# Optimization experiments

Measured on AMD Instinct MI355X. Metric: run time of the kernel, lower is better.

The kernel has to match this reference:

```python
import jax, jax.numpy as jnp
import numpy as np

WS = 7  # window_size

def idct_matrix(N, dtype=jnp.float32):
    # scipy.fftpack.idct type-2 (no norm): y[n] = x[0] + 2*sum_{k>=1} x[k] cos(pi*k*(2n+1)/(2N))
    n = jnp.arange(N, dtype=dtype)[:, None]
    k = jnp.arange(N, dtype=dtype)[None, :]
    M = 2.0 * jnp.cos(jnp.pi * (2.0 * n + 1.0) * k / (2.0 * N))
    return M.at[:, 0].set(1.0)

def setup_inputs() -> dict:
    key = jax.random.key(0)
    k1, k2 = jax.random.split(key)
    B, H, W = 8, 384, 384
    X = jax.random.normal(k1, (B, H, W, WS * WS - 1), dtype=jnp.float32)
    im_zero_freq = jax.random.normal(k2, (B, H, W, 1), dtype=jnp.float32)
    return {"X": X, "im_zero_freq": im_zero_freq}

def reference(X, im_zero_freq):
    B, H, W, _ = X.shape
    ws = WS
    P, Q = H - ws, W - ws  # loop ranges: range(H-ws), range(W-ws)
    # Patch coefficient vector at (i,j): [zero_freq, high_freq...] -> (ws, ws)
    coeff = jnp.concatenate([im_zero_freq[:, :P, :Q, :], X[:, :P, :Q, :]], axis=-1)
    coeff = coeff.reshape(B, P, Q, ws, ws)
    M = idct_matrix(ws).astype(X.dtype)
    # 2D IDCT (axis 1 then axis 2 of each patch) as two small matmuls
    patches = jnp.einsum('nu,mv,bpquv->bpqnm', M, M, coeff)  # [B,P,Q,ws,ws]
    # Overwrite semantics: pixel (y,x) keeps the value from the LAST patch that
    # covered it, i.e. patch (min(y,P-1), min(x,Q-1)). Rows/cols beyond H-2/W-2
    # are never written and stay zero.
    y = jnp.arange(H)
    x = jnp.arange(W)
    i_sel = jnp.minimum(y, P - 1)
    j_sel = jnp.minimum(x, Q - 1)
    dy = y - i_sel  # offset within the selected patch, in [0, ws-1]
    dx = x - j_sel
    out = patches[:, i_sel[:, None], j_sel[None, :], dy[:, None], dx[None, :]]  # [B,H,W]
    valid = (y[:, None] <= H - 2) & (x[None, :] <= W - 2)
    out = jnp.where(valid[None, :, :], out, jnp.zeros((), dtype=out.dtype))
    return out[..., None]  # [B,H,W,1]
```

## Files before the change

kernel.cpp:

```cpp
#include <hip/hip_runtime.h>

#define WS 7
#define BB 8
#define HH 384
#define WW 384
#define PP 377
#define NC 48
#define STRIDE 49
#define NSITE PP
#define NX4 (PP * 12)

__constant__ float d_M[49] = {
    1.0f,  1.9498558244f,  1.8019377358f,  1.5636629649f,  1.2469796037f,  0.8677674782f,  0.4450418679f,
    1.0f,  1.5636629649f,  0.4450418679f, -0.8677674782f, -1.8019377358f, -1.9498558244f, -1.2469796037f,
    1.0f,  0.8677674782f, -1.2469796037f, -1.9498558244f, -0.4450418679f,  1.5636629649f,  1.8019377358f,
    1.0f,  0.0f,          -2.0f,           0.0f,           2.0f,           0.0f,          -2.0f,
    1.0f, -0.8677674782f, -1.2469796037f,  1.9498558244f, -0.4450418679f, -1.5636629649f,  1.8019377358f,
    1.0f, -1.5636629649f,  0.4450418679f,  0.8677674782f, -1.8019377358f,  1.9498558244f, -1.2469796037f,
    1.0f, -1.9498558244f,  1.8019377358f, -1.5636629649f,  1.2469796037f, -0.8677674782f,  0.4450418679f,
};

__global__ __launch_bounds__(384) void idct_row_kernel(
    const float* __restrict__ X,
    const float* __restrict__ zf,
    float* __restrict__ out)
{
    __shared__ float lds[NSITE * STRIDE];
    __shared__ float ldsM[49];

    const int t   = threadIdx.x;
    const int row = blockIdx.x;
    const int y   = row % HH;
    const int b   = row / HH;

    const size_t obase = (size_t)row * WW;

    if (y == HH - 1) { out[obase + t] = 0.0f; return; }

    const int i = min(y, PP - 1);
    const size_t rbase = ((size_t)b * HH + i) * WW;
    const float4* __restrict__ xrow = (const float4*)(X + rbase * NC);

    if (t < 49) ldsM[t] = d_M[t];

    for (int q = t; q < NX4; q += 384) {
        float4 v = xrow[q];
        int j = q / 12;
        int m = q - j * 12;
        float* dst = &lds[j * STRIDE + 1 + 4 * m];
        dst[0] = v.x; dst[1] = v.y; dst[2] = v.z; dst[3] = v.w;
    }
    if (t < NSITE) lds[t * STRIDE] = zf[rbase + t];

    __syncthreads();

    const int x  = t;
    const int j  = min(x, PP - 1);
    const int dx = x - j;
    const int dy = y - i;

    const float* c  = &lds[j * STRIDE];
    const float* wu = &ldsM[dy * 7];
    const float* wv = &ldsM[dx * 7];

    float acc = 0.0f;
#pragma unroll
    for (int u = 0; u < 7; ++u) {
        float s = 0.0f;
#pragma unroll
        for (int v = 0; v < 7; ++v)
            s = fmaf(wv[v], c[u * 7 + v], s);
        acc = fmaf(wu[u], s, acc);
    }

    if (x == WW - 1) acc = 0.0f;
    out[obase + x] = acc;
}

extern "C" void kernel_launch(void* const* d_in, const int* in_sizes, int n_in,
                              void* d_out, int out_size, void* d_ws, size_t ws_size,
                              hipStream_t stream) {
    const float* X  = (const float*)d_in[0];
    const float* zf = (const float*)d_in[1];
    float* out = (float*)d_out;

    idct_row_kernel<<<BB * HH, 384, 0, stream>>>(X, zf, out);
}
```

Before: 340.9 us.

## Compute per-float4 partial dot products in registers instead of staging patches in LDS

Each thread now loads its twelve float4 chunks of the patch row into registers and multiplies them straight away with precomputed 2D IDCT weights (outer product of the row and column weight vectors for dx=0). Only 12 partial sums per site go to LDS instead of the full 49-coefficient patch, which cuts LDS traffic and bank conflicts. The final stage sums the partials per site. The few edge columns where dx>0 fall back to a direct global-memory computation. It adds extra global reads on the edge path and a second barrier.

After: 305.9 us. -10.3%, faster.

```diff
diff --git a/kernel.cpp b/kernel.cpp
--- a/kernel.cpp
+++ b/kernel.cpp
@@ -1,14 +1,10 @@
 #include <hip/hip_runtime.h>
 
-#define WS 7
-#define BB 8
 #define HH 384
 #define WW 384
 #define PP 377
 #define NC 48
-#define STRIDE 49
-#define NSITE PP
-#define NX4 (PP * 12)
+#define NX4R (PP * 12)
 
 __constant__ float d_M[49] = {
     1.0f,  1.9498558244f,  1.8019377358f,  1.5636629649f,  1.2469796037f,  0.8677674782f,  0.4450418679f,
@@ -20,60 +16,84 @@
     1.0f, -1.9498558244f,  1.8019377358f, -1.5636629649f,  1.2469796037f, -0.8677674782f,  0.4450418679f,
 };
 
-__global__ __launch_bounds__(384) void idct_row_kernel(
+__global__ __launch_bounds__(384) void idct_partial_kernel(
     const float* __restrict__ X,
     const float* __restrict__ zf,
     float* __restrict__ out)
 {
-    __shared__ float lds[NSITE * STRIDE];
-    __shared__ float ldsM[49];
+    __shared__ float w49[49];
+    __shared__ float part[PP * 13];
 
     const int t   = threadIdx.x;
     const int row = blockIdx.x;
     const int y   = row % HH;
     const int b   = row / HH;
-
     const size_t obase = (size_t)row * WW;
 
     if (y == HH - 1) { out[obase + t] = 0.0f; return; }
 
-    const int i = min(y, PP - 1);
+    const int i  = min(y, PP - 1);
+    const int dy = y - i;
     const size_t rbase = ((size_t)b * HH + i) * WW;
+
+    if (t < 49) w49[t] = d_M[dy * 7 + t / 7] * d_M[t % 7];
+    __syncthreads();
+
+    const int m  = t % 12;
+    const int s0 = t / 12;
+    const float wa = w49[1 + 4 * m];
+    const float wb = w49[2 + 4 * m];
+    const float wc = w49[3 + 4 * m];
+    const float wd = w49[4 + 4 * m];
+
     const float4* __restrict__ xrow = (const float4*)(X + rbase * NC);
 
-    if (t < 49) ldsM[t] = d_M[t];
-
-    for (int q = t; q < NX4; q += 384) {
-        float4 v = xrow[q];
-        int j = q / 12;
-        int m = q - j * 12;
-        float* dst = &lds[j * STRIDE + 1 + 4 * m];
-        dst[0] = v.x; dst[1] = v.y; dst[2] = v.z; dst[3] = v.w;
+    float4 v[12];
+#pragma unroll
+    for (int k = 0; k < 12; ++k) {
+        int q = t + 384 * k;
+        v[k] = xrow[q < NX4R ? q : (NX4R - 1)];
     }
-    if (t < NSITE) lds[t * STRIDE] = zf[rbase + t];
-
+#pragma unroll
+    for (int k = 0; k < 12; ++k) {
+        int q = t + 384 * k;
+        if (q < NX4R) {
+            float p = fmaf(v[k].x, wa, fmaf(v[k].y, wb, fmaf(v[k].z, wc, v[k].w * wd)));
+            part[(s0 + 32 * k) * 13 + m] = p;
+        }
+    }
     __syncthreads();
 
-    const int x  = t;
-    const int j  = min(x, PP - 1);
-    const int dx = x - j;
-    const int dy = y - i;
+    const int x = t;
+    const int j = min(x, PP - 1);
+    const float zv = zf[rbase + j];
+    float acc;
 
-    const float* c  = &lds[j * STRIDE];
-    const float* wu = &ldsM[dy * 7];
-    const float* wv = &ldsM[dx * 7];
-
-    float acc = 0.0f;
+    if (x < PP) {
+        const float* p = &part[j * 13];
+        float a0 = (p[0] + p[1]) + (p[2] + p[3]);
+        float a1 = (p[4] + p[5]) + (p[6] + p[7]);
+        float a2 = (p[8] + p[9]) + (p[10] + p[11]);
+        acc = zv + (a0 + a1) + a2;
+    } else if (x == WW - 1) {
+        acc = 0.0f;
+    } else {
+        const int dx = x - (PP - 1);
+        const float* __restrict__ c = X + (rbase + (PP - 1)) * NC;
+        acc = 0.0f;
 #pragma unroll
-    for (int u = 0; u < 7; ++u) {
-        float s = 0.0f;
+        for (int u = 0; u < 7; ++u) {
+            float s = 0.0f;
 #pragma unroll
-        for (int v = 0; v < 7; ++v)
-            s = fmaf(wv[v], c[u * 7 + v], s);
-        acc = fmaf(wu[u], s, acc);
+            for (int vv = 0; vv < 7; ++vv) {
+                int n = u * 7 + vv;
+                float cv = (n == 0) ? zv : c[n - 1];
+                s = fmaf(d_M[dx * 7 + vv], cv, s);
+            }
+            acc = fmaf(d_M[dy * 7 + u], s, acc);
+        }
     }
 
-    if (x == WW - 1) acc = 0.0f;
     out[obase + x] = acc;
 }
 
@@ -84,5 +104,5 @@
     const float* zf = (const float*)d_in[1];
     float* out = (float*)d_out;
 
-    idct_row_kernel<<<BB * HH, 384, 0, stream>>>(X, zf, out);
+    idct_partial_kernel<<<8 * HH, 384, 0, stream>>>(X, zf, out);
 }
```
